# Kernel tuning notes

Hardware: AMD Instinct MI355X
Metric: run time of the kernel (lower is better)

Reference implementation:

```python
import jax, jax.numpy as jnp
import numpy as np

N_NODES = 4096
N_EDGES = 262144
D = 128
N_REL = 1000
N_ENT = 50000


def setup_inputs() -> dict:
    key = jax.random.key(0)
    ks = jax.random.split(key, 6)
    x = jax.random.normal(ks[0], (N_NODES, D), dtype=jnp.float32)
    edge_index = jax.random.randint(ks[1], (2, N_EDGES), 0, N_NODES)
    relation_id = jax.random.randint(ks[2], (N_EDGES,), 0, N_REL)
    neg_flag = jax.random.randint(ks[3], (N_EDGES,), 0, 2)
    rel_emb = jax.random.normal(ks[4], (N_REL, D), dtype=jnp.float32)
    entity_emb = jax.random.normal(ks[5], (N_ENT, D), dtype=jnp.float32)
    scale = jnp.ones((N_ENT,), dtype=jnp.float32)
    bias = jnp.zeros((N_ENT,), dtype=jnp.float32)
    return {"x": x, "edge_index": edge_index, "relation_id": relation_id,
            "neg_flag": neg_flag, "rel_emb": rel_emb, "entity_emb": entity_emb,
            "scale": scale, "bias": bias}


def reference(x, edge_index, relation_id, neg_flag, rel_emb, entity_emb, scale, bias):
    src, dst = edge_index[0], edge_index[1]
    # message: gather x_j, TransE tail estimate, sign flip for negated atoms
    neg_coef = 1.0 - 2.0 * neg_flag.astype(x.dtype)           # [E]
    msg = (x[src] + rel_emb[relation_id]) * neg_coef[:, None]  # [E, D]
    # aggregate: scatter-add into target nodes
    aggr_out = jax.ops.segment_sum(msg, dst, num_segments=x.shape[0])  # [N, D]
    # update: residual + bias/scale double-matmul through entity table
    aggr = 0.1 * x + aggr_out                                  # [N, D]
    entity_score = aggr @ entity_emb.T                          # [N, V]
    entity_score = jax.nn.relu(entity_score * scale + bias)
    out = entity_score @ entity_emb                             # [N, D]
    return out
```

## Files before the change

kernel.cpp:

```cpp
#include <hip/hip_runtime.h>
#include <stdint.h>

typedef __attribute__((ext_vector_type(8))) short short8;
typedef __attribute__((ext_vector_type(8))) unsigned short ushort8;
typedef __attribute__((ext_vector_type(4))) float f32x4;
typedef __attribute__((ext_vector_type(16))) float f32x16;
typedef __attribute__((ext_vector_type(2))) unsigned int uint2v;

#define NNODES 4096
#define NEDGES 262144
#define DIM 128
#define NENT 50000
#define NENTP 50048
#define ETILE 32
#define NT32 1563
#define NSPLIT 24

__device__ __forceinline__ unsigned short f2bf(float f) {
  union { __bf16 b; unsigned short u; } c;
  c.b = (__bf16)f;
  return c.u;
}

__global__ __launch_bounds__(256) void k_hist(
    const int* __restrict__ ei, int* __restrict__ cnt)
{
  int e = blockIdx.x * 256 + threadIdx.x;
  atomicAdd(&cnt[ei[NEDGES + e]], 1);
}

__global__ __launch_bounds__(1024) void k_scan(
    const int* __restrict__ cnt, int* __restrict__ off, int* __restrict__ cur)
{
  __shared__ int s[1024];
  int t = threadIdx.x;
  int4 v = reinterpret_cast<const int4*>(cnt)[t];
  int lsum = v.x + v.y + v.z + v.w;
  s[t] = lsum; __syncthreads();
  for (int d = 1; d < 1024; d <<= 1) {
    int a = (t >= d) ? s[t - d] : 0;
    __syncthreads();
    s[t] += a;
    __syncthreads();
  }
  int base = s[t] - lsum;
  int4 o; o.x = base; o.y = base + v.x; o.z = o.y + v.y; o.w = o.z + v.z;
  reinterpret_cast<int4*>(off)[t] = o;
  reinterpret_cast<int4*>(cur)[t] = o;
  if (t == 1023) off[4096] = base + lsum;
}

__global__ __launch_bounds__(256) void k_place(
    const int* __restrict__ ei, const int* __restrict__ rid,
    const int* __restrict__ nf, int* __restrict__ cur, int* __restrict__ sorted)
{
  int e = blockIdx.x * 256 + threadIdx.x;
  int dst = ei[NEDGES + e];
  int pos = atomicAdd(&cur[dst], 1);
  sorted[pos] = ei[e] | (rid[e] << 12) | (nf[e] << 22);
}

__global__ __launch_bounds__(256) void k_aggr(
    const int* __restrict__ off, const int* __restrict__ sorted,
    const float* __restrict__ x, const float* __restrict__ rel,
    unsigned short* __restrict__ q)
{
  __shared__ float sAcc[8 * 132];
  const int n = blockIdx.x;
  const int t = threadIdx.x;
  const int slot = t >> 5;
  const int c = t & 31;
  const int b = off[n], eN = off[n + 1];
  float4 acc = make_float4(0.f, 0.f, 0.f, 0.f);
  for (int i = b + slot; i < eN; i += 8) {
    int p = sorted[i];
    float4 xv = reinterpret_cast<const float4*>(x)[(p & 4095) * 32 + c];
    float4 rv = reinterpret_cast<const float4*>(rel)[((p >> 12) & 1023) * 32 + c];
    float sgn = (p & (1 << 22)) ? -1.f : 1.f;
    acc.x += sgn * (xv.x + rv.x);
    acc.y += sgn * (xv.y + rv.y);
    acc.z += sgn * (xv.z + rv.z);
    acc.w += sgn * (xv.w + rv.w);
  }
  *reinterpret_cast<float4*>(&sAcc[slot * 132 + c * 4]) = acc;
  __syncthreads();
  if (t < 128) {
    float s = 0.f;
#pragma unroll
    for (int k = 0; k < 8; ++k) s += sAcc[k * 132 + t];
    q[n * DIM + t] = f2bf(0.1f * x[n * DIM + t] + s);
  }
}

__global__ __launch_bounds__(256) void k_prep(
    const float* __restrict__ ent, const float* __restrict__ scale,
    unsigned short* __restrict__ ebf, unsigned short* __restrict__ etbf)
{
  __shared__ float sT[64 * 133];
  const int t = threadIdx.x;
  const int e0 = blockIdx.x * 64;
#pragma unroll
  for (int i = 0; i < 8; ++i) {
    int idx = i * 256 + t;
    int e = idx >> 5;
    int c4 = idx & 31;
    float4 v = make_float4(0.f, 0.f, 0.f, 0.f);
    float sc = 0.f;
    if (e0 + e < NENT) {
      v = reinterpret_cast<const float4*>(ent)[(e0 + e) * 32 + c4];
      sc = scale[e0 + e];
    }
    *reinterpret_cast<float4*>(&sT[e * 133 + c4 * 4]) = v;
    ushort4 bq;
    bq.x = f2bf(v.x * sc); bq.y = f2bf(v.y * sc);
    bq.z = f2bf(v.z * sc); bq.w = f2bf(v.w * sc);
    *reinterpret_cast<ushort4*>(&ebf[(e0 + e) * 128 + c4 * 4]) = bq;
  }
  __syncthreads();
  const int lane = t & 63;
  const int w = t >> 6;
  const int dl = lane >> 3;
  const int el = (lane & 7) * 8;
#pragma unroll
  for (int it = 0; it < 4; ++it) {
    int d = it * 32 + w * 8 + dl;
    ushort8 buf;
#pragma unroll
    for (int j = 0; j < 8; ++j) buf[j] = f2bf(sT[(el + j) * 133 + d]);
    *reinterpret_cast<ushort8*>(&etbf[d * NENTP + e0 + el]) = buf;
  }
}


__device__ __forceinline__ void gll16(const void* g, void* l) {
  __builtin_amdgcn_global_load_lds(
      (const __attribute__((address_space(1))) unsigned int*)g,
      (__attribute__((address_space(3))) unsigned int*)l, 16, 0, 0);
}

__device__ __forceinline__ unsigned cvtpk(float lo, float hi) {
  unsigned r;
  asm("v_cvt_pk_bf16_f32 %0, %1, %2" : "=v"(r) : "v"(lo), "v"(hi));
  return r;
}

__global__ __launch_bounds__(256, 3) void k_flash(
    const unsigned short* __restrict__ qg,
    const unsigned short* __restrict__ ebf,
    const unsigned short* __restrict__ etbf,
    const float* __restrict__ bias,
    float* __restrict__ out)
{
  __shared__ __align__(16) unsigned short sE[2][ETILE * 128];
  __shared__ __align__(16) unsigned short sET[2][128 * ETILE];
  __shared__ __align__(16) float sBias[2][ETILE];

  const int t = threadIdx.x;
  const int w = t >> 6;
  const int lane = t & 63;
  const int l31 = lane & 31;
  const int hi = lane >> 5;

  const int m0 = blockIdx.x * 128;
  const int tile_lo = (blockIdx.y * NT32) / NSPLIT;
  const int tile_hi = ((blockIdx.y + 1) * NT32) / NSPLIT;

  const int cE = (((t & 15) ^ ((t >> 4) & 15))) * 8;
  const int rE = t >> 4;
  const int cT = (((t & 3) ^ ((t >> 2) & 3))) * 8;
  const int rT = t >> 2;

  short8 qf[8];
  {
    const unsigned short* qrow = qg + (size_t)(m0 + w * 32 + l31) * DIM + hi * 8;
#pragma unroll
    for (int kk = 0; kk < 8; ++kk)
      qf[kk] = *reinterpret_cast<const short8*>(qrow + kk * 16);
  }

  f32x16 accO[4];
#pragma unroll
  for (int td = 0; td < 4; ++td)
#pragma unroll
    for (int r = 0; r < 16; ++r) accO[td][r] = 0.f;

  {
    const int vt = tile_lo * ETILE;
#pragma unroll
    for (int i = 0; i < 2; ++i)
      gll16(ebf + (size_t)(vt + i * 16 + rE) * DIM + cE, &sE[0][(i * 256 + t) * 8]);
#pragma unroll
    for (int i = 0; i < 2; ++i)
      gll16(etbf + (size_t)(i * 64 + rT) * NENTP + vt + cT, &sET[0][(i * 256 + t) * 8]);
    if (t < ETILE) sBias[0][t] = (vt + t < NENT) ? bias[vt + t] : 0.f;
  }
  __syncthreads();

  int cur = 0;
  for (int tile = tile_lo; tile < tile_hi; ++tile) {
    if (tile + 1 < tile_hi) {
      const int vt = (tile + 1) * ETILE;
#pragma unroll
      for (int i = 0; i < 2; ++i)
        gll16(ebf + (size_t)(vt + i * 16 + rE) * DIM + cE,
              &sE[cur ^ 1][(i * 256 + t) * 8]);
#pragma unroll
      for (int i = 0; i < 2; ++i)
        gll16(etbf + (size_t)(i * 64 + rT) * NENTP + vt + cT,
              &sET[cur ^ 1][(i * 256 + t) * 8]);
      if (t < ETILE) sBias[cur ^ 1][t] = (vt + t < NENT) ? bias[vt + t] : 0.f;
    }

    const unsigned short* sEc = sE[cur];
    const float* sb = sBias[cur];
    f32x16 accST;
#pragma unroll
    for (int r = 0; r < 16; ++r) accST[r] = 0.f;

    __builtin_amdgcn_s_setprio(1);
#pragma unroll
    for (int kk = 0; kk < 8; ++kk) {
      const int col = ((kk * 2 + hi) ^ (l31 & 15)) * 8;
      short8 a = *reinterpret_cast<const short8*>(&sEc[l31 * 128 + col]);
      accST = __builtin_amdgcn_mfma_f32_32x32x16_bf16(a, qf[kk], accST, 0, 0, 0);
    }
    __builtin_amdgcn_s_setprio(0);

    short8 F[2];
    {
      float p[16];
#pragma unroll
      for (int g = 0; g < 4; ++g) {
        f32x4 b4 = *reinterpret_cast<const f32x4*>(&sb[g * 8 + hi * 4]);
#pragma unroll
        for (int j = 0; j < 4; ++j)
          p[g * 4 + j] = fmaxf(accST[g * 4 + j] + b4[j], 0.f);
      }
      unsigned wr[8];
#pragma unroll
      for (int c2 = 0; c2 < 8; ++c2) wr[c2] = cvtpk(p[2 * c2], p[2 * c2 + 1]);
      uint2v r02 = __builtin_amdgcn_permlane32_swap(wr[0], wr[2], false, false);
      uint2v r13 = __builtin_amdgcn_permlane32_swap(wr[1], wr[3], false, false);
      uint2v r46 = __builtin_amdgcn_permlane32_swap(wr[4], wr[6], false, false);
      uint2v r57 = __builtin_amdgcn_permlane32_swap(wr[5], wr[7], false, false);
      union { unsigned u[4]; short8 s; } f0, f1;
      f0.u[0] = r02[0]; f0.u[1] = r13[0]; f0.u[2] = r02[1]; f0.u[3] = r13[1];
      f1.u[0] = r46[0]; f1.u[1] = r57[0]; f1.u[2] = r46[1]; f1.u[3] = r57[1];
      F[0] = f0.s;
      F[1] = f1.s;
    }

    const unsigned short* sTc = sET[cur];
    __builtin_amdgcn_s_setprio(1);
#pragma unroll
    for (int ke = 0; ke < 2; ++ke) {
      const int col0 = (ke * 2 + hi);
#pragma unroll
      for (int td = 0; td < 4; ++td) {
        const int d = td * 32 + l31;
        const int col = (col0 ^ (l31 & 3)) * 8;
        short8 bT = *reinterpret_cast<const short8*>(&sTc[d * ETILE + col]);
        accO[td] = __builtin_amdgcn_mfma_f32_32x32x16_bf16(F[ke], bT, accO[td], 0, 0, 0);
      }
    }
    __builtin_amdgcn_s_setprio(0);

    __syncthreads();
    cur ^= 1;
  }

#pragma unroll
  for (int td = 0; td < 4; ++td) {
#pragma unroll
    for (int r = 0; r < 16; ++r) {
      int qrow = (r & 3) + 8 * (r >> 2) + 4 * hi;
      int row = m0 + w * 32 + qrow;
      int col = td * 32 + l31;
      atomicAdd(&out[(size_t)row * DIM + col], accO[td][r]);
    }
  }
}

extern "C" void kernel_launch(void* const* d_in, const int* in_sizes, int n_in,
                              void* d_out, int out_size, void* d_ws, size_t ws_size,
                              hipStream_t stream) {
  const float* x     = (const float*)d_in[0];
  const int*   ei    = (const int*)d_in[1];
  const int*   rid   = (const int*)d_in[2];
  const int*   nf    = (const int*)d_in[3];
  const float* rel   = (const float*)d_in[4];
  const float* ent   = (const float*)d_in[5];
  const float* scale = (const float*)d_in[6];
  const float* bias  = (const float*)d_in[7];
  float* out = (float*)d_out;

  char* ws = (char*)d_ws;
  int*            cnt    = (int*)(ws + 0);
  int*            off    = (int*)(ws + (16u << 10));
  int*            cur    = (int*)(ws + (36u << 10));
  int*            sorted = (int*)(ws + (64u << 10));
  unsigned short* qb     = (unsigned short*)(ws + (1344u << 10));
  unsigned short* ebf    = (unsigned short*)(ws + (2560u << 10));
  unsigned short* etbf   = (unsigned short*)(ws + (2560u << 10) + (size_t)NENTP * DIM * 2);

  hipMemsetAsync(cnt, 0, 4096 * sizeof(int), stream);
  hipMemsetAsync(d_out, 0, (size_t)out_size * sizeof(float), stream);
  k_prep<<<NENTP / 64, 256, 0, stream>>>(ent, scale, ebf, etbf);
  k_hist<<<NEDGES / 256, 256, 0, stream>>>(ei, cnt);
  k_scan<<<1, 1024, 0, stream>>>(cnt, off, cur);
  k_place<<<NEDGES / 256, 256, 0, stream>>>(ei, rid, nf, cur, sorted);
  k_aggr<<<NNODES, 256, 0, stream>>>(off, sorted, x, rel, qb);
  k_flash<<<dim3(NNODES / 128, NSPLIT), 256, 0, stream>>>(qb, ebf, etbf, bias, out);
}
```

Before: 284.0 us.

## Fuse histogram into prep kernel, split score MFMA chain, change sET swizzle

Folds the edge-destination histogram into the entity-prep kernel by appending extra blocks, which removes one kernel launch. In the flash kernel, the score MFMA dependency chain is split into two independent accumulators that are summed before ReLU, so the matrix unit can overlap them. The XOR swizzle key for the transposed entity tile is changed on both the write and read side to reduce LDS bank conflicts. The two-accumulator split costs extra registers, and the prep and histogram blocks now share one grid.

Measured after the change: 270.0 us. 1.05x faster.

```diff
diff --git a/kernel.cpp b/kernel.cpp
--- a/kernel.cpp
+++ b/kernel.cpp
@@ -12,6 +12,7 @@
 #define DIM 128
 #define NENT 50000
 #define NENTP 50048
+#define PREPB 782
 #define ETILE 32
 #define NT32 1563
 #define NSPLIT 24
@@ -20,13 +21,6 @@
   union { __bf16 b; unsigned short u; } c;
   c.b = (__bf16)f;
   return c.u;
-}
-
-__global__ __launch_bounds__(256) void k_hist(
-    const int* __restrict__ ei, int* __restrict__ cnt)
-{
-  int e = blockIdx.x * 256 + threadIdx.x;
-  atomicAdd(&cnt[ei[NEDGES + e]], 1);
 }
 
 __global__ __launch_bounds__(1024) void k_scan(
@@ -94,8 +88,14 @@
 
 __global__ __launch_bounds__(256) void k_prep(
     const float* __restrict__ ent, const float* __restrict__ scale,
-    unsigned short* __restrict__ ebf, unsigned short* __restrict__ etbf)
-{
+    unsigned short* __restrict__ ebf, unsigned short* __restrict__ etbf,
+    const int* __restrict__ ei, int* __restrict__ cnt)
+{
+  if (blockIdx.x >= PREPB) {
+    int e = (blockIdx.x - PREPB) * 256 + threadIdx.x;
+    atomicAdd(&cnt[ei[NEDGES + e]], 1);
+    return;
+  }
   __shared__ float sT[64 * 133];
   const int t = threadIdx.x;
   const int e0 = blockIdx.x * 64;
@@ -167,7 +167,7 @@
 
   const int cE = (((t & 15) ^ ((t >> 4) & 15))) * 8;
   const int rE = t >> 4;
-  const int cT = (((t & 3) ^ ((t >> 2) & 3))) * 8;
+  const int cT = (((t & 3) ^ ((t >> 4) & 3))) * 8;
   const int rT = t >> 2;
 
   short8 qf[8];
@@ -213,16 +213,19 @@
 
     const unsigned short* sEc = sE[cur];
     const float* sb = sBias[cur];
-    f32x16 accST;
-#pragma unroll
-    for (int r = 0; r < 16; ++r) accST[r] = 0.f;
+    f32x16 accA, accB;
+#pragma unroll
+    for (int r = 0; r < 16; ++r) { accA[r] = 0.f; accB[r] = 0.f; }
 
     __builtin_amdgcn_s_setprio(1);
 #pragma unroll
-    for (int kk = 0; kk < 8; ++kk) {
-      const int col = ((kk * 2 + hi) ^ (l31 & 15)) * 8;
-      short8 a = *reinterpret_cast<const short8*>(&sEc[l31 * 128 + col]);
-      accST = __builtin_amdgcn_mfma_f32_32x32x16_bf16(a, qf[kk], accST, 0, 0, 0);
+    for (int kk = 0; kk < 4; ++kk) {
+      const int colA = ((kk * 4 + hi) ^ (l31 & 15)) * 8;
+      const int colB = ((kk * 4 + 2 + hi) ^ (l31 & 15)) * 8;
+      short8 a0 = *reinterpret_cast<const short8*>(&sEc[l31 * 128 + colA]);
+      short8 a1 = *reinterpret_cast<const short8*>(&sEc[l31 * 128 + colB]);
+      accA = __builtin_amdgcn_mfma_f32_32x32x16_bf16(a0, qf[2 * kk], accA, 0, 0, 0);
+      accB = __builtin_amdgcn_mfma_f32_32x32x16_bf16(a1, qf[2 * kk + 1], accB, 0, 0, 0);
     }
     __builtin_amdgcn_s_setprio(0);
 
@@ -234,7 +237,7 @@
         f32x4 b4 = *reinterpret_cast<const f32x4*>(&sb[g * 8 + hi * 4]);
 #pragma unroll
         for (int j = 0; j < 4; ++j)
-          p[g * 4 + j] = fmaxf(accST[g * 4 + j] + b4[j], 0.f);
+          p[g * 4 + j] = fmaxf(accA[g * 4 + j] + accB[g * 4 + j] + b4[j], 0.f);
       }
       unsigned wr[8];
 #pragma unroll
@@ -251,14 +254,14 @@
     }
 
     const unsigned short* sTc = sET[cur];
+    const int keyT = (l31 >> 2) & 3;
     __builtin_amdgcn_s_setprio(1);
 #pragma unroll
     for (int ke = 0; ke < 2; ++ke) {
-      const int col0 = (ke * 2 + hi);
+      const int col = ((ke * 2 + hi) ^ keyT) * 8;
 #pragma unroll
       for (int td = 0; td < 4; ++td) {
         const int d = td * 32 + l31;
-        const int col = (col0 ^ (l31 & 3)) * 8;
         short8 bT = *reinterpret_cast<const short8*>(&sTc[d * ETILE + col]);
         accO[td] = __builtin_amdgcn_mfma_f32_32x32x16_bf16(F[ke], bT, accO[td], 0, 0, 0);
       }
@@ -305,8 +308,7 @@
 
   hipMemsetAsync(cnt, 0, 4096 * sizeof(int), stream);
   hipMemsetAsync(d_out, 0, (size_t)out_size * sizeof(float), stream);
-  k_prep<<<NENTP / 64, 256, 0, stream>>>(ent, scale, ebf, etbf);
-  k_hist<<<NEDGES / 256, 256, 0, stream>>>(ei, cnt);
+  k_prep<<<PREPB + NEDGES / 256, 256, 0, stream>>>(ent, scale, ebf, etbf, ei, cnt);
   k_scan<<<1, 1024, 0, stream>>>(cnt, off, cur);
   k_place<<<NEDGES / 256, 256, 0, stream>>>(ei, rid, nf, cur, sorted);
   k_aggr<<<NNODES, 256, 0, stream>>>(off, sorted, x, rel, qb);
```
